# Optimization experiments

Hardware: AMD Instinct MI355X
Metric: run time of the kernel (lower is better)

Reference implementation:

```python
import jax, jax.numpy as jnp
import numpy as np

BS = 2; D = 256; NH = 8; NL = 4; NP = 4; WS = 7; DFF = 1024
SHAPES = [(92, 92), (46, 46), (23, 23), (12, 12)]
LEN = sum(h * w for h, w in SHAPES)  # 11253
DH = D // NH


def _layer_norm(x, g, b):
    mu = jnp.mean(x, -1, keepdims=True)
    var = jnp.var(x, -1, keepdims=True)
    return (x - mu) * jax.lax.rsqrt(var + 1e-5) * g + b


def _bilinear(v_l, loc, H_, W_):
    # v_l: (N, nh, H_*W_, d); loc: (N, Lq, nh, P, 2) normalized in [0,1] (x, y)
    N, Lq, nh, P, _ = loc.shape
    x = loc[..., 0] * W_ - 0.5  # grid_sample align_corners=False convention
    y = loc[..., 1] * H_ - 0.5
    x0f = jnp.floor(x); y0f = jnp.floor(y)
    tx = (x - x0f).transpose(0, 2, 1, 3)  # (N, nh, Lq, P)
    ty = (y - y0f).transpose(0, 2, 1, 3)
    x0 = x0f.astype(jnp.int32).transpose(0, 2, 1, 3)
    y0 = y0f.astype(jnp.int32).transpose(0, 2, 1, 3)

    def g(yi, xi):
        valid = ((xi >= 0) & (xi < W_) & (yi >= 0) & (yi < H_)).astype(v_l.dtype)
        idx = (jnp.clip(yi, 0, H_ - 1) * W_ + jnp.clip(xi, 0, W_ - 1)).reshape(N, nh, Lq * P)
        out = jnp.take_along_axis(v_l, idx[..., None], axis=2).reshape(N, nh, Lq, P, -1)
        return out * valid[..., None]

    return (g(y0, x0) * ((1 - tx) * (1 - ty))[..., None]
            + g(y0, x0 + 1) * (tx * (1 - ty))[..., None]
            + g(y0 + 1, x0) * ((1 - tx) * ty)[..., None]
            + g(y0 + 1, x0 + 1) * (tx * ty)[..., None])


def setup_inputs() -> dict:
    key = jax.random.key(0)
    ks = jax.random.split(key, 20)
    s = 0.02
    inp = {}
    inp['src'] = jax.random.normal(ks[0], (BS, LEN, D), jnp.float32)
    inp['pos'] = jax.random.normal(ks[1], (BS, LEN, D), jnp.float32)
    inp['reference_points'] = jax.random.uniform(ks[2], (BS, LEN, NL, 2), jnp.float32)
    c = WS // 2
    ys, xs = jnp.meshgrid(jnp.arange(WS) - c, jnp.arange(WS) - c, indexing='ij')
    inp['window_grid'] = jnp.stack([xs, ys], -1).reshape(WS * WS, 2).astype(jnp.float32)
    for l, (h, w) in enumerate(SHAPES):
        inp[f'mask{l}'] = jax.random.normal(ks[3 + l], (BS, 1, h, w), jnp.float32)
    inp['spatial_shapes'] = jnp.array(SHAPES, jnp.int32)
    starts = np.cumsum([0] + [h * w for h, w in SHAPES])[:NL]
    inp['level_start_index'] = jnp.array(starts, jnp.int32)
    # parse_mask: Conv2d(1, n_heads, 1) per level -> per-head scale + bias
    inp['pm_w'] = jax.random.normal(ks[7], (NL, NH), jnp.float32) * s
    inp['pm_b'] = jax.random.normal(ks[8], (NL, NH), jnp.float32) * s
    inp['Wv'] = jax.random.normal(ks[9], (D, D), jnp.float32) * s
    inp['bv'] = jnp.zeros((D,), jnp.float32)
    inp['Wo'] = jax.random.normal(ks[10], (D, D), jnp.float32) * s
    inp['bo'] = jnp.zeros((D,), jnp.float32)
    inp['ln1_g'] = jnp.ones((D,), jnp.float32)
    inp['ln1_b'] = jnp.zeros((D,), jnp.float32)
    inp['W1'] = jax.random.normal(ks[11], (D, DFF), jnp.float32) * s
    inp['b1'] = jnp.zeros((DFF,), jnp.float32)
    inp['W2'] = jax.random.normal(ks[12], (DFF, D), jnp.float32) * s
    inp['b2'] = jnp.zeros((D,), jnp.float32)
    inp['ln2_g'] = jnp.ones((D,), jnp.float32)
    inp['ln2_b'] = jnp.zeros((D,), jnp.float32)
    return inp


def reference(src, pos, reference_points, window_grid, mask0, mask1, mask2, mask3,
              spatial_shapes, level_start_index, pm_w, pm_b, Wv, bv, Wo, bo,
              ln1_g, ln1_b, W1, b1, W2, b2, ln2_g, ln2_b):
    masks = [mask0, mask1, mask2, mask3]
    p = WS // 2
    offs, samp = [], []
    for l, (H_, W_) in enumerate(SHAPES):
        # 1x1 conv from 1 -> NH channels
        m = masks[l] * pm_w[l][None, :, None, None] + pm_b[l][None, :, None, None]  # (BS,NH,H,W)
        mp = jnp.pad(m, ((0, 0), (0, 0), (p, p), (p, p)))
        # unfold: (BS, NH, WS*WS, H*W), kernel positions row-major
        patches = jnp.stack([mp[:, :, i:i + H_, j:j + W_] for i in range(WS) for j in range(WS)], axis=2)
        patches = patches.reshape(BS, NH, WS * WS, H_ * W_).transpose(0, 1, 3, 2)  # (BS,NH,HW,WS^2)
        vals, idx = jax.lax.top_k(patches, NP)  # (BS,NH,HW,NP)
        off = window_grid[idx]  # (BS,NH,HW,NP,2)
        offs.append(off.transpose(0, 2, 1, 3, 4))   # (BS,HW,NH,NP,2)
        samp.append(vals.transpose(0, 2, 1, 3))     # (BS,HW,NH,NP)
    offsets = jnp.concatenate(offs, axis=1)       # (BS,LEN,NH,NP,2)
    pred_sampled = jnp.concatenate(samp, axis=1)  # (BS,LEN,NH,NP)

    # MSDeformAttn (encoder mode: external offsets + mask-derived attention logits)
    value = (src @ Wv + bv).reshape(BS, LEN, NH, DH)
    attn = jax.nn.softmax(
        jnp.broadcast_to(pred_sampled[:, :, :, None, :], (BS, LEN, NH, NL, NP)).reshape(BS, LEN, NH, NL * NP),
        axis=-1).reshape(BS, LEN, NH, NL, NP)
    norm = jnp.array([[w, h] for h, w in SHAPES], jnp.float32)  # (NL, 2) as (W, H)
    loc = reference_points[:, :, None, :, None, :] + offsets[:, :, :, None, :, :] / norm[None, None, None, :, None, :]

    out = jnp.zeros((BS, LEN, NH, DH), src.dtype)
    s0 = 0
    for l, (H_, W_) in enumerate(SHAPES):
        v_l = value[:, s0:s0 + H_ * W_].transpose(0, 2, 1, 3)  # (BS,NH,HW,DH)
        sampled = _bilinear(v_l, loc[:, :, :, l], H_, W_)       # (BS,NH,LEN,NP,DH)
        out = out + jnp.einsum('nhqpd,nqhp->nqhd', sampled, attn[:, :, :, l])
        s0 += H_ * W_
    attn_out = out.reshape(BS, LEN, D) @ Wo + bo

    x = _layer_norm(src + attn_out, ln1_g, ln1_b)
    x2 = jax.nn.relu(x @ W1 + b1) @ W2 + b2
    return _layer_norm(x + x2, ln2_g, ln2_b)
```

## Files before the change

### kernel.cpp

```cpp
#include <hip/hip_runtime.h>
#include <cstddef>
#include <cstdint>

#define LEN_T 11253
#define TOK   22506
#define NHEADS 8
#define DMODEL 256

typedef __attribute__((ext_vector_type(8))) short short8;
typedef __attribute__((ext_vector_type(4))) float f32x4;

__device__ __forceinline__ unsigned short f2bf(float f) {
  union { float f; unsigned u; } v; v.f = f;
  unsigned r = v.u + 0x7fffu + ((v.u >> 16) & 1u);
  return (unsigned short)(r >> 16);
}
__device__ __forceinline__ float bfhi2f(unsigned u) {
  union { unsigned u; float f; } v; v.u = u & 0xffff0000u; return v.f;
}
__device__ __forceinline__ float bflo2f(unsigned u) {
  union { unsigned u; float f; } v; v.u = u << 16; return v.f;
}
__device__ __forceinline__ float bf2f(unsigned short s) {
  union { unsigned u; float f; } v; v.u = (unsigned)s << 16; return v.f;
}
__device__ __forceinline__ void gld_lds16(const void* g, void* l) {
  __builtin_amdgcn_global_load_lds(
      (const __attribute__((address_space(1))) void*)g,
      (__attribute__((address_space(3))) void*)l, 16, 0, 0);
}

__device__ __forceinline__ void ins4(float v, int ji,
    float& t0, float& t1, float& t2, float& t3,
    int& i0, int& i1, int& i2, int& i3)
{
  bool a0 = v > t0, a1 = v > t1, a2 = v > t2, a3 = v > t3;
  t3 = a3 ? (a2 ? t2 : v) : t3;  i3 = a3 ? (a2 ? i2 : ji) : i3;
  t2 = a2 ? (a1 ? t1 : v) : t2;  i2 = a2 ? (a1 ? i1 : ji) : i2;
  t1 = a1 ? (a0 ? t0 : v) : t1;  i1 = a1 ? (a0 ? i0 : ji) : i1;
  t0 = a0 ? v : t0;              i0 = a0 ? ji : i0;
}

__global__ __launch_bounds__(256) void pre_kernel(
    const float* __restrict__ m0, const float* __restrict__ m1,
    const float* __restrict__ m2, const float* __restrict__ m3,
    const float* __restrict__ pm_w, const float* __restrict__ pm_b,
    const float* __restrict__ Wv, const float* __restrict__ Wo,
    const float* __restrict__ W1, const float* __restrict__ W2,
    unsigned short* __restrict__ Wv_t, unsigned short* __restrict__ Wo_t,
    unsigned short* __restrict__ W1_t, unsigned short* __restrict__ W2_t,
    unsigned* __restrict__ offp, float* __restrict__ attw)
{
  int blk = blockIdx.x;
  if (blk >= 704) {
    int cb = blk - 704;
    const float* W; unsigned short* Bt; int lk, ln, base;
    if (cb < 64)       { W = Wv; Bt = Wv_t; lk = 8;  ln = 8;  base = cb; }
    else if (cb < 128) { W = Wo; Bt = Wo_t; lk = 8;  ln = 8;  base = cb - 64; }
    else if (cb < 384) { W = W1; Bt = W1_t; lk = 8;  ln = 10; base = cb - 128; }
    else               { W = W2; Bt = W2_t; lk = 10; ln = 8;  base = cb - 384; }
    int i4 = (base * 256 + threadIdx.x) * 4;
    int n  = i4 >> lk;
    int k  = i4 & ((1 << lk) - 1);
    ushort4 o;
    o.x = f2bf(W[((size_t)(k + 0) << ln) + n]);
    o.y = f2bf(W[((size_t)(k + 1) << ln) + n]);
    o.z = f2bf(W[((size_t)(k + 2) << ln) + n]);
    o.w = f2bf(W[((size_t)(k + 3) << ln) + n]);
    *(ushort4*)(Bt + i4) = o;
    return;
  }
  int t = blk * 256 + threadIdx.x;
  if (t >= TOK * NHEADS) return;
  int h  = t & 7;
  int bq = t >> 3;
  int b  = bq / LEN_T;
  int q  = bq - b * LEN_T;
  int l, H_, W_;
  const float* mk;
  if (q < 8464)       { l = 0; H_ = 92; W_ = 92; mk = m0; }
  else if (q < 10580) { l = 1; H_ = 46; W_ = 46; mk = m1; }
  else if (q < 11109) { l = 2; H_ = 23; W_ = 23; mk = m2; }
  else                { l = 3; H_ = 12; W_ = 12; mk = m3; }
  int st = (l == 0) ? 0 : (l == 1) ? 8464 : (l == 2) ? 10580 : 11109;
  int pos = q - st;
  int rr = pos / W_;
  int cc = pos - rr * W_;
  float w  = pm_w[l * NHEADS + h];
  float bb = pm_b[l * NHEADS + h];
  const float* mp = mk + (size_t)b * H_ * W_;

  float t0=-1e30f,t1=-1e30f,t2=-1e30f,t3=-1e30f;
  int   i0=0,i1=0,i2=0,i3=0;
  for (int i = 0; i < 7; ++i) {
    int yy = rr + i - 3;
    #pragma unroll
    for (int j = 0; j < 7; ++j) {
      int xx = cc + j - 3;
      float v = 0.f;
      if (yy >= 0 && yy < H_ && xx >= 0 && xx < W_)
        v = mp[(size_t)yy * W_ + xx] * w + bb;
      ins4(v, j | (i << 4), t0, t1, t2, t3, i0, i1, i2, i3);
    }
  }
  float e1 = __expf(t1 - t0);
  float e2 = __expf(t2 - t0);
  float e3 = __expf(t3 - t0);
  float inv = 1.f / (4.f * (1.f + e1 + e2 + e3));
  float4 wout; wout.x = inv; wout.y = e1 * inv; wout.z = e2 * inv; wout.w = e3 * inv;
  *(float4*)(attw + (size_t)t * 4) = wout;
  offp[t] = (unsigned)i0 | ((unsigned)i1 << 8)
          | ((unsigned)i2 << 16) | ((unsigned)i3 << 24);
}

__global__ __launch_bounds__(256) void sample_kernel(
    const unsigned short* __restrict__ Vb, const float* __restrict__ refpts,
    const unsigned* __restrict__ offp, const float* __restrict__ attw,
    unsigned short* __restrict__ outp)
{
  __shared__ int4  sidx[4][128];
  __shared__ float4 swgt[4][128];
  const int wv   = threadIdx.x >> 6;
  const int lane = threadIdx.x & 63;
  const int bx = blockIdx.x & 7, by = blockIdx.x >> 3;
  const int nb = bx * 703 + min(bx, 3) + by;
  const int blk = nb * 4 + wv;
  const bool ok = blk < TOK;

  if (ok) {
    const int b = (blk >= LEN_T) ? 1 : 0;
    const float* rp = refpts + (size_t)blk * 8;
    #pragma unroll
    for (int e = 0; e < 2; ++e) {
      int t = lane * 2 + e;
      int h = t & 7, lp = t >> 3;
      int l = lp >> 2, p = lp & 3;
      unsigned pb = (offp[(size_t)blk * 8 + h] >> (8 * p)) & 0xffu;
      float ox = (float)(int)(pb & 15u) - 3.f;
      float oy = (float)(int)(pb >> 4)  - 3.f;
      float aw = attw[((size_t)blk * 8 + h) * 4 + p];
      int H_ = (l == 0) ? 92 : (l == 1) ? 46 : (l == 2) ? 23 : 12;
      int st = (l == 0) ? 0  : (l == 1) ? 8464 : (l == 2) ? 10580 : 11109;
      float xx = rp[2 * l]     * (float)H_ - 0.5f + ox;
      float yy = rp[2 * l + 1] * (float)H_ - 0.5f + oy;
      float x0f = floorf(xx), y0f = floorf(yy);
      float tx = xx - x0f, ty = yy - y0f;
      int x0 = (int)x0f, y0 = (int)y0f;
      int base = b * LEN_T + st;
      float wc[4] = {(1.f - tx) * (1.f - ty), tx * (1.f - ty),
                     (1.f - tx) * ty,         tx * ty};
      int4 idx; float4 wg;
      int xs[4] = {x0, x0 + 1, x0, x0 + 1};
      int ys[4] = {y0, y0, y0 + 1, y0 + 1};
      int   id[4]; float wgt[4];
      #pragma unroll
      for (int c = 0; c < 4; ++c) {
        int xi = xs[c], yi = ys[c];
        bool v_ = (xi >= 0) & (xi < H_) & (yi >= 0) & (yi < H_);
        id[c]  = base + min(max(yi, 0), H_ - 1) * H_ + min(max(xi, 0), H_ - 1);
        wgt[c] = v_ ? aw * wc[c] : 0.f;
      }
      idx.x = id[0]; idx.y = id[1]; idx.z = id[2]; idx.w = id[3];
      wg.x = wgt[0]; wg.y = wgt[1]; wg.z = wgt[2]; wg.w = wgt[3];
      sidx[wv][t] = idx;
      swgt[wv][t] = wg;
    }
  }
  __syncthreads();

  if (ok) {
    const int h = lane >> 3, dg = lane & 7;
    const unsigned short* vb = Vb + h * 32 + dg * 4;
    f32x4 acc = {0.f, 0.f, 0.f, 0.f};

    uint2  u[2][8];
    float4 wg[2][2];

    #pragma unroll
    for (int j = 0; j < 2; ++j) {
      int4 idx  = sidx[wv][j * 8 + h];
      wg[0][j]  = swgt[wv][j * 8 + h];
      u[0][j*4+0] = *(const uint2*)(vb + (size_t)idx.x * DMODEL);
      u[0][j*4+1] = *(const uint2*)(vb + (size_t)idx.y * DMODEL);
      u[0][j*4+2] = *(const uint2*)(vb + (size_t)idx.z * DMODEL);
      u[0][j*4+3] = *(const uint2*)(vb + (size_t)idx.w * DMODEL);
    }
    #pragma unroll
    for (int bt = 0; bt < 8; ++bt) {
      const int cur = bt & 1, nxt = cur ^ 1;
      if (bt < 7) {
        #pragma unroll
        for (int j = 0; j < 2; ++j) {
          int lp = (bt + 1) * 2 + j;
          int4 idx   = sidx[wv][lp * 8 + h];
          wg[nxt][j] = swgt[wv][lp * 8 + h];
          u[nxt][j*4+0] = *(const uint2*)(vb + (size_t)idx.x * DMODEL);
          u[nxt][j*4+1] = *(const uint2*)(vb + (size_t)idx.y * DMODEL);
          u[nxt][j*4+2] = *(const uint2*)(vb + (size_t)idx.z * DMODEL);
          u[nxt][j*4+3] = *(const uint2*)(vb + (size_t)idx.w * DMODEL);
        }
      }
      #pragma unroll
      for (int j = 0; j < 2; ++j) {
        const float4 w4 = wg[cur][j];
        const uint2 u0 = u[cur][j*4+0], u1 = u[cur][j*4+1];
        const uint2 u2 = u[cur][j*4+2], u3 = u[cur][j*4+3];
        acc.x += w4.x * bflo2f(u0.x) + w4.y * bflo2f(u1.x) + w4.z * bflo2f(u2.x) + w4.w * bflo2f(u3.x);
        acc.y += w4.x * bfhi2f(u0.x) + w4.y * bfhi2f(u1.x) + w4.z * bfhi2f(u2.x) + w4.w * bfhi2f(u3.x);
        acc.z += w4.x * bflo2f(u0.y) + w4.y * bflo2f(u1.y) + w4.z * bflo2f(u2.y) + w4.w * bflo2f(u3.y);
        acc.w += w4.x * bfhi2f(u0.y) + w4.y * bfhi2f(u1.y) + w4.z * bfhi2f(u2.y) + w4.w * bfhi2f(u3.y);
      }
    }
    uint2 o;
    o.x = (unsigned)f2bf(acc.x) | ((unsigned)f2bf(acc.y) << 16);
    o.y = (unsigned)f2bf(acc.z) | ((unsigned)f2bf(acc.w) << 16);
    *(uint2*)(outp + (size_t)blk * DMODEL + h * 32 + dg * 4) = o;
  }
}

template<int EPI, bool AF32, int KC>
__global__ __launch_bounds__(256, 2) void gemm_bres(
    const void* __restrict__ Aptr, const short* __restrict__ Bt,
    const float* __restrict__ bias, const float* __restrict__ res,
    const unsigned short* __restrict__ resb,
    const float* __restrict__ lng, const float* __restrict__ lnb,
    float* __restrict__ C, unsigned short* __restrict__ Cb,
    int M, int N)
{
  constexpr int K = KC * 256;
  constexpr int NBUF = (KC > 1) ? 2 : 1;
  __shared__ short As[NBUF][64 * 256] __attribute__((aligned(16)));
  __shared__ float2 lnred[64][4];
  const int tid  = threadIdx.x;
  const int w    = tid >> 6;
  const int lane = tid & 63;
  const int row0 = blockIdx.x * 64;
  const int wn   = blockIdx.y * 256 + w * 64;
  const int colq = lane & 15, quad = lane >> 4;
  const int kq8  = quad * 8;

  short8 bq[8][4];
  auto loadB = [&](int c) {
    #pragma unroll
    for (int kc = 0; kc < 8; ++kc)
      #pragma unroll
      for (int nt = 0; nt < 4; ++nt)
        bq[kc][nt] = *(const short8*)(Bt + (size_t)(wn + nt * 16 + colq) * K
                                         + c * 256 + kc * 32 + kq8);
  };

  f32x4 acc[4][4];
  #pragma unroll
  for (int i = 0; i < 4; ++i)
    #pragma unroll
    for (int j = 0; j < 4; ++j) acc[i][j] = (f32x4){0.f, 0.f, 0.f, 0.f};

  const int rA   = min(row0 + (tid >> 2), M - 1);
  const int csw8 = (((tid & 3) ^ ((tid >> 3) & 3)) << 3);
  const float* Af = (const float*)Aptr;
  const short* Ab = (const short*)Aptr;
  const size_t abase = (size_t)rA * K;

  auto stageChunk = [&](int c, int nbuf) {
    #pragma unroll
    for (int kb = 0; kb < 8; ++kb) {
      const int gcol = c * 256 + kb * 32 + csw8;
      if constexpr (AF32) {
        const float* ap = Af + abase + gcol;
        float4 f0 = *(const float4*)ap;
        float4 f1 = *(const float4*)(ap + 4);
        uint4 u;
        u.x = (unsigned)f2bf(f0.x) | ((unsigned)f2bf(f0.y) << 16);
        u.y = (unsigned)f2bf(f0.z) | ((unsigned)f2bf(f0.w) << 16);
        u.z = (unsigned)f2bf(f1.x) | ((unsigned)f2bf(f1.y) << 16);
        u.w = (unsigned)f2bf(f1.z) | ((unsigned)f2bf(f1.w) << 16);
        *(uint4*)(As[nbuf] + kb * 2048 + (size_t)tid * 8) = u;
      } else {
        gld_lds16(Ab + abase + gcol, As[nbuf] + kb * 2048 + (size_t)tid * 8);
      }
    }
  };

  const int rsw = (colq >> 1) & 3;
  const int rdo = ((quad ^ rsw) << 3);

  stageChunk(0, 0);
  loadB(0);
  __syncthreads();
  int buf = 0;
  #pragma unroll
  for (int c = 0; c < KC; ++c) {
    if (c + 1 < KC) stageChunk(c + 1, buf ^ 1);
    if (c > 0) loadB(c);
    #pragma unroll
    for (int kb = 0; kb < 8; ++kb) {
      short8 af[4];
      #pragma unroll
      for (int mt = 0; mt < 4; ++mt)
        af[mt] = *(const short8*)(As[buf] + kb * 2048
                                  + (size_t)(mt * 16 + colq) * 32 + rdo);
      #pragma unroll
      for (int mt = 0; mt < 4; ++mt)
        #pragma unroll
        for (int nt = 0; nt < 4; ++nt)
          acc[mt][nt] = __builtin_amdgcn_mfma_f32_16x16x32_bf16(
              af[mt], bq[kb][nt], acc[mt][nt], 0, 0, 0);
    }
    __syncthreads();
    buf ^= 1;
  }

  float bia[4];
  #pragma unroll
  for (int nt = 0; nt < 4; ++nt) bia[nt] = bias[wn + nt * 16 + colq];

  if constexpr (EPI == 1 || EPI == 3) {
    #pragma unroll
    for (int mt = 0; mt < 4; ++mt) {
      #pragma unroll
      for (int r = 0; r < 4; ++r) {
        int lrow = mt * 16 + quad * 4 + r;
        int rowc = min(row0 + lrow, M - 1);
        float s = 0.f, sq = 0.f;
        #pragma unroll
        for (int nt = 0; nt < 4; ++nt) {
          float rv;
          if constexpr (EPI == 1)
            rv = res[(size_t)rowc * 256 + wn + nt * 16 + colq];
          else
            rv = bf2f(resb[(size_t)rowc * 256 + wn + nt * 16 + colq]);
          float f = acc[mt][nt][r] + bia[nt] + rv;
          acc[mt][nt][r] = f;
          s += f; sq += f * f;
        }
        #pragma unroll
        for (int off = 1; off < 16; off <<= 1) {
          s  += __shfl_xor(s,  off, 64);
          sq += __shfl_xor(sq, off, 64);
        }
        if (colq == 0) lnred[lrow][w] = (float2){s, sq};
      }
    }
    __syncthreads();
    #pragma unroll
    for (int mt = 0; mt < 4; ++mt) {
      #pragma unroll
      for (int r = 0; r < 4; ++r) {
        int lrow = mt * 16 + quad * 4 + r;
        int row  = row0 + lrow;
        if (row >= M) continue;
        float2 p0 = lnred[lrow][0], p1 = lnred[lrow][1];
        float2 p2 = lnred[lrow][2], p3 = lnred[lrow][3];
        float mu  = (p0.x + p1.x + p2.x + p3.x) * (1.f / 256.f);
        float var = (p0.y + p1.y + p2.y + p3.y) * (1.f / 256.f) - mu * mu;
        float rs  = rsqrtf(var + 1e-5f);
        #pragma unroll
        for (int nt = 0; nt < 4; ++nt) {
          int col = wn + nt * 16 + colq;
          float o = (acc[mt][nt][r] - mu) * rs * lng[col] + lnb[col];
          if constexpr (EPI == 1)
            Cb[(size_t)row * 256 + col] = f2bf(o);
          else
            C[(size_t)row * 256 + col] = o;
        }
      }
    }
  } else {
    #pragma unroll
    for (int mt = 0; mt < 4; ++mt) {
      #pragma unroll
      for (int r = 0; r < 4; ++r) {
        int row = row0 + mt * 16 + quad * 4 + r;
        if (row < M) {
          #pragma unroll
          for (int nt = 0; nt < 4; ++nt) {
            float f = acc[mt][nt][r] + bia[nt];
            if constexpr (EPI == 2) f = fmaxf(f, 0.f);
            Cb[(size_t)row * N + wn + nt * 16 + colq] = f2bf(f);
          }
        }
      }
    }
  }
}

extern "C" void kernel_launch(void* const* d_in, const int* in_sizes, int n_in,
                              void* d_out, int out_size, void* d_ws, size_t ws_size,
                              hipStream_t stream)
{
  const float* src    = (const float*)d_in[0];
  const float* refpts = (const float*)d_in[2];
  const float* m0   = (const float*)d_in[4];
  const float* m1   = (const float*)d_in[5];
  const float* m2   = (const float*)d_in[6];
  const float* m3   = (const float*)d_in[7];
  const float* pm_w = (const float*)d_in[10];
  const float* pm_b = (const float*)d_in[11];
  const float* Wv   = (const float*)d_in[12];
  const float* bv   = (const float*)d_in[13];
  const float* Wo   = (const float*)d_in[14];
  const float* bo   = (const float*)d_in[15];
  const float* ln1g = (const float*)d_in[16];
  const float* ln1b = (const float*)d_in[17];
  const float* W1   = (const float*)d_in[18];
  const float* b1   = (const float*)d_in[19];
  const float* W2   = (const float*)d_in[20];
  const float* b2   = (const float*)d_in[21];
  const float* ln2g = (const float*)d_in[22];
  const float* ln2b = (const float*)d_in[23];
  float* out = (float*)d_out;
  char*  w   = (char*)d_ws;

  unsigned short* Vb      = (unsigned short*)(w);
  unsigned short* attnpre = (unsigned short*)(w + 11523072);
  unsigned short* h1      = (unsigned short*)(w + 23046144);
  char*           tail    = w + 69138432;
  float*          attw    = (float*)(tail);
  unsigned*       offp    = (unsigned*)(tail + 2880768);
  unsigned short* Wv_t    = (unsigned short*)(tail + 3600960);
  unsigned short* Wo_t    = (unsigned short*)(tail + 3732032);
  unsigned short* W1_t    = (unsigned short*)(tail + 3863104);
  unsigned short* W2_t    = (unsigned short*)(tail + 4387392);
  unsigned short* x_bf    = attnpre;

  pre_kernel<<<dim3(1344), 256, 0, stream>>>(
      m0, m1, m2, m3, pm_w, pm_b, Wv, Wo, W1, W2,
      Wv_t, Wo_t, W1_t, W2_t, offp, attw);

  gemm_bres<0, true, 1><<<dim3(352, 1), 256, 0, stream>>>(
      src, (const short*)Wv_t, bv, nullptr, nullptr, nullptr, nullptr,
      nullptr, Vb, TOK, 256);

  sample_kernel<<<dim3(5627), 256, 0, stream>>>(
      Vb, refpts, offp, attw, attnpre);

  gemm_bres<1, false, 1><<<dim3(352, 1), 256, 0, stream>>>(
      attnpre, (const short*)Wo_t, bo, src, nullptr, ln1g, ln1b,
      nullptr, x_bf, TOK, 256);

  gemm_bres<2, false, 1><<<dim3(352, 4), 256, 0, stream>>>(
      x_bf, (const short*)W1_t, b1, nullptr, nullptr, nullptr, nullptr,
      nullptr, h1, TOK, 1024);

  gemm_bres<3, false, 4><<<dim3(352, 1), 256, 0, stream>>>(
      h1, (const short*)W2_t, b2, nullptr, x_bf, ln2g, ln2b,
      out, nullptr, TOK, 256);
}
```

Before: 315.4 us.

## Stage GEMM B tiles through LDS with per-32-K double buffering

The GEMM no longer holds a whole 256-wide K chunk of B in registers (bq[8][4]). It now streams both A and B through small double-buffered LDS tiles, one 32-wide K slice per iteration, using direct global-to-LDS loads for B. This cuts register pressure and shared-memory footprint, which may allow more occupancy and overlap, at the cost of one barrier per 32-K step instead of per 256-K chunk. Separately, the deformable sampling loop gains sched_barrier fences so the prefetch loads stay ahead of the FMA work.

Measured after the change: 289.2 us. -8.3%, faster.

```diff
diff --git a/kernel.cpp b/kernel.cpp
--- a/kernel.cpp
+++ b/kernel.cpp
@@ -6,6 +6,8 @@
 #define TOK   22506
 #define NHEADS 8
 #define DMODEL 256
+
+#define SBAR() __builtin_amdgcn_sched_barrier(0)
 
 typedef __attribute__((ext_vector_type(8))) short short8;
 typedef __attribute__((ext_vector_type(4))) float f32x4;
@@ -185,6 +187,7 @@
       u[0][j*4+2] = *(const uint2*)(vb + (size_t)idx.z * DMODEL);
       u[0][j*4+3] = *(const uint2*)(vb + (size_t)idx.w * DMODEL);
     }
+    SBAR();
     #pragma unroll
     for (int bt = 0; bt < 8; ++bt) {
       const int cur = bt & 1, nxt = cur ^ 1;
@@ -200,6 +203,7 @@
           u[nxt][j*4+3] = *(const uint2*)(vb + (size_t)idx.w * DMODEL);
         }
       }
+      SBAR();
       #pragma unroll
       for (int j = 0; j < 2; ++j) {
         const float4 w4 = wg[cur][j];
@@ -227,27 +231,18 @@
     float* __restrict__ C, unsigned short* __restrict__ Cb,
     int M, int N)
 {
-  constexpr int K = KC * 256;
-  constexpr int NBUF = (KC > 1) ? 2 : 1;
-  __shared__ short As[NBUF][64 * 256] __attribute__((aligned(16)));
+  constexpr int K  = KC * 256;
+  constexpr int NK = KC * 8;
+  __shared__ short As[2][64 * 32]  __attribute__((aligned(16)));
+  __shared__ short Bs[2][256 * 32] __attribute__((aligned(16)));
   __shared__ float2 lnred[64][4];
   const int tid  = threadIdx.x;
   const int w    = tid >> 6;
   const int lane = tid & 63;
-  const int row0 = blockIdx.x * 64;
-  const int wn   = blockIdx.y * 256 + w * 64;
+  const int row0  = blockIdx.x * 64;
+  const int ncol0 = blockIdx.y * 256;
+  const int wn    = ncol0 + w * 64;
   const int colq = lane & 15, quad = lane >> 4;
-  const int kq8  = quad * 8;
-
-  short8 bq[8][4];
-  auto loadB = [&](int c) {
-    #pragma unroll
-    for (int kc = 0; kc < 8; ++kc)
-      #pragma unroll
-      for (int nt = 0; nt < 4; ++nt)
-        bq[kc][nt] = *(const short8*)(Bt + (size_t)(wn + nt * 16 + colq) * K
-                                         + c * 256 + kc * 32 + kq8);
-  };
 
   f32x4 acc[4][4];
   #pragma unroll
@@ -256,56 +251,67 @@
     for (int j = 0; j < 4; ++j) acc[i][j] = (f32x4){0.f, 0.f, 0.f, 0.f};
 
   const int rA   = min(row0 + (tid >> 2), M - 1);
-  const int csw8 = (((tid & 3) ^ ((tid >> 3) & 3)) << 3);
+  const int ksw8 = (((tid & 3) ^ ((tid >> 3) & 3)) << 3);
   const float* Af = (const float*)Aptr;
   const short* Ab = (const short*)Aptr;
   const size_t abase = (size_t)rA * K;
-
-  auto stageChunk = [&](int c, int nbuf) {
-    #pragma unroll
-    for (int kb = 0; kb < 8; ++kb) {
-      const int gcol = c * 256 + kb * 32 + csw8;
-      if constexpr (AF32) {
-        const float* ap = Af + abase + gcol;
-        float4 f0 = *(const float4*)ap;
-        float4 f1 = *(const float4*)(ap + 4);
-        uint4 u;
-        u.x = (unsigned)f2bf(f0.x) | ((unsigned)f2bf(f0.y) << 16);
-        u.y = (unsigned)f2bf(f0.z) | ((unsigned)f2bf(f0.w) << 16);
-        u.z = (unsigned)f2bf(f1.x) | ((unsigned)f2bf(f1.y) << 16);
-        u.w = (unsigned)f2bf(f1.z) | ((unsigned)f2bf(f1.w) << 16);
-        *(uint4*)(As[nbuf] + kb * 2048 + (size_t)tid * 8) = u;
-      } else {
-        gld_lds16(Ab + abase + gcol, As[nbuf] + kb * 2048 + (size_t)tid * 8);
-      }
+  const int nrowB = ncol0 + w * 64 + (lane >> 2);
+
+  float4 pA0, pA1;
+  auto loadA_f32 = [&](int kb) {
+    const float* ap = Af + abase + kb * 32 + ksw8;
+    pA0 = *(const float4*)ap;
+    pA1 = *(const float4*)(ap + 4);
+  };
+  auto writeA_f32 = [&](int nbuf) {
+    uint4 u;
+    u.x = (unsigned)f2bf(pA0.x) | ((unsigned)f2bf(pA0.y) << 16);
+    u.y = (unsigned)f2bf(pA0.z) | ((unsigned)f2bf(pA0.w) << 16);
+    u.z = (unsigned)f2bf(pA1.x) | ((unsigned)f2bf(pA1.y) << 16);
+    u.w = (unsigned)f2bf(pA1.z) | ((unsigned)f2bf(pA1.w) << 16);
+    *(uint4*)(As[nbuf] + (size_t)tid * 8) = u;
+  };
+  auto stageA_bf = [&](int kb, int nbuf) {
+    gld_lds16(Ab + abase + kb * 32 + ksw8, As[nbuf] + (size_t)tid * 8);
+  };
+  auto stageB = [&](int kb, int nbuf) {
+    const int kg = kb * 32;
+    #pragma unroll
+    for (int j = 0; j < 4; ++j) {
+      gld_lds16(Bt + (size_t)(nrowB + j * 16) * K + kg + ksw8,
+                Bs[nbuf] + (size_t)(w * 2048 + j * 512) + lane * 8);
     }
   };
 
   const int rsw = (colq >> 1) & 3;
   const int rdo = ((quad ^ rsw) << 3);
 
-  stageChunk(0, 0);
-  loadB(0);
+  if constexpr (AF32) { loadA_f32(0); stageB(0, 0); writeA_f32(0); }
+  else                { stageA_bf(0, 0); stageB(0, 0); }
   __syncthreads();
   int buf = 0;
-  #pragma unroll
-  for (int c = 0; c < KC; ++c) {
-    if (c + 1 < KC) stageChunk(c + 1, buf ^ 1);
-    if (c > 0) loadB(c);
-    #pragma unroll
-    for (int kb = 0; kb < 8; ++kb) {
-      short8 af[4];
-      #pragma unroll
-      for (int mt = 0; mt < 4; ++mt)
-        af[mt] = *(const short8*)(As[buf] + kb * 2048
-                                  + (size_t)(mt * 16 + colq) * 32 + rdo);
-      #pragma unroll
-      for (int mt = 0; mt < 4; ++mt)
-        #pragma unroll
-        for (int nt = 0; nt < 4; ++nt)
-          acc[mt][nt] = __builtin_amdgcn_mfma_f32_16x16x32_bf16(
-              af[mt], bq[kb][nt], acc[mt][nt], 0, 0, 0);
-    }
+  for (int kb = 0; kb < NK; ++kb) {
+    const bool more = (kb + 1 < NK);
+    if constexpr (AF32) {
+      if (more) { stageB(kb + 1, buf ^ 1); loadA_f32(kb + 1); }
+    } else {
+      if (more) { stageA_bf(kb + 1, buf ^ 1); stageB(kb + 1, buf ^ 1); }
+    }
+    short8 af[4], bf[4];
+    #pragma unroll
+    for (int mt = 0; mt < 4; ++mt)
+      af[mt] = *(const short8*)(As[buf] + (size_t)(mt * 16 + colq) * 32 + rdo);
+    #pragma unroll
+    for (int nt = 0; nt < 4; ++nt)
+      bf[nt] = *(const short8*)(Bs[buf] + (size_t)(w * 2048 + nt * 512)
+                                + colq * 32 + rdo);
+    #pragma unroll
+    for (int mt = 0; mt < 4; ++mt)
+      #pragma unroll
+      for (int nt = 0; nt < 4; ++nt)
+        acc[mt][nt] = __builtin_amdgcn_mfma_f32_16x16x32_bf16(
+            af[mt], bf[nt], acc[mt][nt], 0, 0, 0);
+    if constexpr (AF32) { if (more) writeA_f32(buf ^ 1); }
     __syncthreads();
     buf ^= 1;
   }
```
